# Optimization experiments

Hardware: AMD Instinct MI355X
Metric: run time of the kernel (lower is better)

The kernel has to match this reference:

```python
import jax, jax.numpy as jnp
import numpy as np

B, T, C = 4, 2048, 1024
H = 16
HD = C // H


def setup_inputs() -> dict:
    key = jax.random.key(0)
    k1, k2, k3 = jax.random.split(key, 3)
    x = jax.random.normal(k1, (B, T, C), dtype=jnp.float32)
    w_qkv = jax.random.normal(k2, (C, 3 * C), dtype=jnp.float32) * (C ** -0.5)
    w_proj = jax.random.normal(k3, (C, C), dtype=jnp.float32) * (C ** -0.5)
    b_proj = jnp.zeros((C,), dtype=jnp.float32)
    return {"x": x, "w_qkv": w_qkv, "w_proj": w_proj, "b_proj": b_proj}


def reference(x, w_qkv, w_proj, b_proj):
    Bd, Td, Cd = x.shape
    scale = HD ** -0.5
    qkv = x @ w_qkv  # [B,T,3C]
    q, k, v = jnp.split(qkv, 3, axis=-1)
    # [B,H,T,HD]
    q = q.reshape(Bd, Td, H, HD).transpose(0, 2, 1, 3)
    k = k.reshape(Bd, Td, H, HD).transpose(0, 2, 1, 3)
    v = v.reshape(Bd, Td, H, HD).transpose(0, 2, 1, 3)
    att = jnp.einsum('bhqd,bhkd->bhqk', q, k) * scale
    causal = jnp.triu(jnp.ones((Td, Td), dtype=bool), k=1)
    att = jnp.where(causal, -jnp.inf, att)
    att = jax.nn.softmax(att, axis=-1)
    y = jnp.einsum('bhqk,bhkd->bhqd', att, v)
    y = y.transpose(0, 2, 1, 3).reshape(Bd, Td, Cd)
    return y @ w_proj + b_proj
```

## Files before the change

kernel.cpp:

```cpp
#include <hip/hip_runtime.h>

typedef unsigned short u16;
typedef __attribute__((ext_vector_type(8))) short short8;
typedef __attribute__((ext_vector_type(4))) short short4v;
typedef __attribute__((ext_vector_type(4))) float floatx4;
typedef __attribute__((ext_vector_type(4))) unsigned short ushort4v;

#define B_ 4
#define T_ 2048
#define C_ 1024
#define H_ 16
#define HD_ 64

template <bool V> struct BC { static constexpr bool value = V; };
template <int N> struct ICN { static constexpr int v = N; };

static __device__ __forceinline__ u16 f2bf(float f) {
  union { float f; unsigned int i; } c; c.f = f;
  unsigned int u = c.i;
  return (u16)((u + 0x7FFFu + ((u >> 16) & 1u)) >> 16);
}
static __device__ __forceinline__ unsigned pk2(float lo, float hi) {
  union { float f; unsigned u; } a, b; a.f = hi; b.f = lo;
  return __builtin_amdgcn_perm(a.u, b.u, 0x07060302u);
}
static __device__ __forceinline__ unsigned pk2r(float lo, float hi) {
  return (unsigned)f2bf(lo) | ((unsigned)f2bf(hi) << 16);
}

static __device__ __forceinline__ void gload16(const u16* g, u16* l) {
  __builtin_amdgcn_global_load_lds(
      (const __attribute__((address_space(1))) unsigned int*)(g),
      (__attribute__((address_space(3))) unsigned int*)(l), 16, 0, 0);
}

__global__ __launch_bounds__(256) void prep_k(const float* __restrict__ x,
                                              const float* __restrict__ w_qkv,
                                              const float* __restrict__ w_proj,
                                              u16* __restrict__ xbf,
                                              u16* __restrict__ wqkvT,
                                              u16* __restrict__ wprojT) {
  const int bid = blockIdx.x;
  if (bid < 8192) {
    const int i = bid * 256 + threadIdx.x;
    const float4 f = ((const float4*)x)[i];
    ushort4v o;
    o.x = f2bf(f.x); o.y = f2bf(f.y); o.z = f2bf(f.z); o.w = f2bf(f.w);
    *(ushort4v*)(xbf + (size_t)i * 4) = o;
    return;
  }
  __shared__ u16 tile[32][33];
  const float* in;
  u16* out;
  int R, Cc, tb;
  if (bid < 11264) {
    in = w_qkv; out = wqkvT; R = C_; Cc = 3 * C_; tb = bid - 8192;
  } else {
    in = w_proj; out = wprojT; R = C_; Cc = C_; tb = bid - 11264;
  }
  const int tpr = Cc / 32;
  const int bx = (tb % tpr) * 32;
  const int by = (tb / tpr) * 32;
  const int tx = threadIdx.x & 31;
  const int ty = threadIdx.x >> 5;
  #pragma unroll
  for (int i = ty; i < 32; i += 8)
    tile[i][tx] = f2bf(in[(size_t)(by + i) * Cc + bx + tx]);
  __syncthreads();
  #pragma unroll
  for (int i = ty; i < 32; i += 8)
    out[(size_t)(bx + i) * R + by + tx] = tile[tx][i];
}

template <int MODE>
__global__ __launch_bounds__(512, 2) void gemm8p(const u16* __restrict__ A,
                                                 const u16* __restrict__ Bt,
                                                 u16* __restrict__ outb,
                                                 u16* __restrict__ outv,
                                                 float* __restrict__ outf,
                                                 const float* __restrict__ bias,
                                                 int M, int N, int K) {
  __shared__ __align__(16) u16 lds[49152];
  const int bid = blockIdx.x;
  const int xcd = bid & 7;
  const int loc = bid >> 3;
  const int tM = (xcd * 8 + (loc & 7)) * 128;
  const int tN = (loc >> 3) * 256;
  const int tid = threadIdx.x;
  const int wave = tid >> 6;
  const int lane = tid & 63;
  const int lr = lane & 15;
  const int quad = lane >> 4;
  const int wm = wave >> 2;
  const int wn = wave & 3;
  const int csw = (lr >> 1) & 3;
  const int arow = wave * 16 + (lane >> 2);
  const int skofs = ((lane & 3) ^ ((lane >> 3) & 3)) * 8;
  const int KT = K >> 5;

  const floatx4 zf = {0.f, 0.f, 0.f, 0.f};
  floatx4 acc[4][4];
  #pragma unroll
  for (int i = 0; i < 4; i++)
    #pragma unroll
    for (int j = 0; j < 4; j++) acc[i][j] = zf;

  auto stage = [&](int t) {
    const int buf = t & 3;
    const int kk = t * 32;
    gload16(A + (size_t)(tM + arow) * K + kk + skofs,
            &lds[buf * 4096 + wave * 512]);
    gload16(Bt + (size_t)(tN + arow) * K + kk + skofs,
            &lds[16384 + buf * 8192 + wave * 512]);
    gload16(Bt + (size_t)(tN + 128 + arow) * K + kk + skofs,
            &lds[16384 + buf * 8192 + 4096 + wave * 512]);
  };

  auto ktile = [&](int t, auto VM) {
    const int buf = t & 3;
    const u16* lA = &lds[buf * 4096];
    const u16* lB = &lds[16384 + buf * 8192];
    short8 af[4], bfr[4];
    #pragma unroll
    for (int mt = 0; mt < 4; mt++)
      af[mt] = *(const short8*)(&lA[(wm * 64 + mt * 16 + lr) * 32 + ((quad ^ csw) * 8)]);
    #pragma unroll
    for (int nt = 0; nt < 4; nt++)
      bfr[nt] = *(const short8*)(&lB[(wn * 64 + nt * 16 + lr) * 32 + ((quad ^ csw) * 8)]);
    if (t + 3 < KT) stage(t + 3);
    asm volatile("s_waitcnt lgkmcnt(0)" ::: "memory");
    __builtin_amdgcn_sched_barrier(0);
    __builtin_amdgcn_s_setprio(1);
    #pragma unroll
    for (int mt = 0; mt < 4; mt++)
      #pragma unroll
      for (int nt = 0; nt < 4; nt++)
        acc[mt][nt] = __builtin_amdgcn_mfma_f32_16x16x32_bf16(af[mt], bfr[nt],
                                                              acc[mt][nt], 0, 0, 0);
    __builtin_amdgcn_s_setprio(0);
    __builtin_amdgcn_sched_barrier(0);
    constexpr int vm = decltype(VM)::v;
    if constexpr (vm == 6)
      asm volatile("s_waitcnt vmcnt(6)\n\ts_barrier" ::: "memory");
    else if constexpr (vm == 3)
      asm volatile("s_waitcnt vmcnt(3)\n\ts_barrier" ::: "memory");
    else if constexpr (vm == 0)
      asm volatile("s_waitcnt vmcnt(0)\n\ts_barrier" ::: "memory");
  };

  stage(0); stage(1); stage(2);
  asm volatile("s_waitcnt vmcnt(6)\n\ts_barrier" ::: "memory");

  for (int t = 0; t < KT - 3; t++) ktile(t, ICN<6>{});
  ktile(KT - 3, ICN<3>{});
  ktile(KT - 2, ICN<0>{});
  ktile(KT - 1, ICN<-1>{});

  if constexpr (MODE == 1) {
    if (tN >= 2 * C_) {
      asm volatile("s_barrier" ::: "memory");
      #pragma unroll
      for (int mt = 0; mt < 4; mt++) {
        const int t0 = wm * 64 + mt * 16 + quad * 4;
        #pragma unroll
        for (int nt = 0; nt < 4; nt++) {
          const int vrow = wn * 64 + nt * 16 + lr;
          u16* p = &lds[vrow * 128 + (((t0 >> 3) ^ (vrow & 7)) * 8) + (t0 & 7)];
          *(unsigned*)(p)     = pk2r(acc[mt][nt][0], acc[mt][nt][1]);
          *(unsigned*)(p + 2) = pk2r(acc[mt][nt][2], acc[mt][nt][3]);
        }
      }
      asm volatile("s_waitcnt lgkmcnt(0)\n\ts_barrier" ::: "memory");
      const int b = tM >> 11;
      const int t0b = tM & (T_ - 1);
      const int h0 = (tN - 2 * C_) >> 6;
      u16* vb = outv + (size_t)(b * H_ + h0) * HD_ * T_;
      #pragma unroll
      for (int i = 0; i < 8; i++) {
        const int lin = tid + i * 512;
        const int row = lin >> 4;
        const int chv = lin & 15;
        const short8 v = *(const short8*)(&lds[row * 128 + ((chv ^ (row & 7)) * 8)]);
        *(short8*)(vb + (size_t)row * T_ + t0b + chv * 8) = v;
      }
      return;
    }
    #pragma unroll
    for (int mt = 0; mt < 4; mt++) {
      const int m0 = tM + wm * 64 + mt * 16 + quad * 4;
      #pragma unroll
      for (int nt = 0; nt < 4; nt++) {
        const int n = tN + wn * 64 + nt * 16 + lr;
        #pragma unroll
        for (int r = 0; r < 4; r++)
          outb[(size_t)(m0 + r) * N + n] = f2bf(acc[mt][nt][r]);
      }
    }
  } else {
    #pragma unroll
    for (int mt = 0; mt < 4; mt++) {
      const int m0 = tM + wm * 64 + mt * 16 + quad * 4;
      #pragma unroll
      for (int nt = 0; nt < 4; nt++) {
        const int n = tN + wn * 64 + nt * 16 + lr;
        const float bv = bias[n];
        #pragma unroll
        for (int r = 0; r < 4; r++)
          __builtin_nontemporal_store(acc[mt][nt][r] + bv,
                                      &outf[(size_t)(m0 + r) * N + n]);
      }
    }
  }
}

__global__ __launch_bounds__(256, 4) void attn_k(const u16* __restrict__ qkv,
                                                 const u16* __restrict__ vt,
                                                 u16* __restrict__ y) {
  __shared__ __align__(16) u16 Ks[64 * 64];
  __shared__ __align__(16) u16 Vs[64 * 64];
  const int bid = blockIdx.x;
  const int s = bid >> 3;
  const int qp = s >> 3;
  const int bh = ((s & 7) << 3) | (bid & 7);
  const int b = bh >> 4, h = bh & 15;
  const int tid = threadIdx.x;
  const int wave = tid >> 6;
  const int lane = tid & 63;
  const int lr = lane & 15;
  const int quad = lane >> 4;
  const int qtA = qp, qtB = 31 - qp;

  const int srow = lane >> 3;
  const int skofs = ((lane & 7) ^ ((lane >> 3) & 7)) * 8;
  const int gsw = lr & 7;

  const size_t RS = 3 * C_;
  const u16* qcol = qkv + (size_t)b * T_ * RS + h * HD_;
  const u16* kcol = qcol + C_;

  const size_t qrA = (size_t)(qtA * 64 + wave * 16 + lr) * RS;
  const size_t qrB = (size_t)(qtB * 64 + wave * 16 + lr) * RS;
  const short8 aq0A = *(const short8*)(qcol + qrA + quad * 8);
  const short8 aq1A = *(const short8*)(qcol + qrA + 32 + quad * 8);
  const short8 aq0B = *(const short8*)(qcol + qrB + quad * 8);
  const short8 aq1B = *(const short8*)(qcol + qrB + 32 + quad * 8);

  const floatx4 zf = {0.f, 0.f, 0.f, 0.f};
  const float C1 = 0.125f * 1.44269504f;
  const float C2 = -16.0f * 1.44269504f;
  const short8 vones = {16256, 16256, 16256, 16256, 16256, 16256, 16256, 16256};

  floatx4 accA[4], accB[4];
  floatx4 accSA = zf, accSB = zf;
  #pragma unroll
  for (int i = 0; i < 4; i++) { accA[i] = zf; accB[i] = zf; }

  auto stage = [&](int kt) {
    __syncthreads();
    #pragma unroll
    for (int j = 0; j < 2; j++) {
      const int seg = wave * 2 + j;
      const int row = seg * 8 + srow;
      gload16(kcol + (size_t)(kt * 64 + row) * RS + skofs, &Ks[seg * 512]);
      gload16(vt + ((size_t)bh * HD_ + row) * T_ + kt * 64 + skofs, &Vs[seg * 512]);
    }
    __syncthreads();
  };

  auto core = [&](auto WA, auto DA, auto DB) {
    constexpr bool wA = decltype(WA)::value;
    constexpr bool dA = decltype(DA)::value;
    constexpr bool dB = decltype(DB)::value;
    float peA[4][4], peB[4][4];
    #pragma unroll
    for (int nt = 0; nt < 4; nt++) {
      const short8 bk0 =
          *(const short8*)(&Ks[(nt * 16 + lr) * 64 + ((quad ^ gsw) * 8)]);
      const short8 bk1 =
          *(const short8*)(&Ks[(nt * 16 + lr) * 64 + (((quad + 4) ^ gsw) * 8)]);
      {
        floatx4 st = __builtin_amdgcn_mfma_f32_16x16x32_bf16(
            bk1, aq1B,
            __builtin_amdgcn_mfma_f32_16x16x32_bf16(bk0, aq0B, zf, 0, 0, 0),
            0, 0, 0);
        #pragma unroll
        for (int r = 0; r < 4; r++) {
          float pe = __builtin_amdgcn_exp2f(fmaf(st[r], C1, C2));
          if constexpr (dB)
            if (nt * 16 + quad * 4 + r > wave * 16 + lr) pe = 0.f;
          peB[nt][r] = pe;
        }
      }
      if constexpr (wA) {
        floatx4 st = __builtin_amdgcn_mfma_f32_16x16x32_bf16(
            bk1, aq1A,
            __builtin_amdgcn_mfma_f32_16x16x32_bf16(bk0, aq0A, zf, 0, 0, 0),
            0, 0, 0);
        #pragma unroll
        for (int r = 0; r < 4; r++) {
          float pe = __builtin_amdgcn_exp2f(fmaf(st[r], C1, C2));
          if constexpr (dA)
            if (nt * 16 + quad * 4 + r > wave * 16 + lr) pe = 0.f;
          peA[nt][r] = pe;
        }
      }
    }

    short8 pB[2], pA[2];
    #pragma unroll
    for (int h2 = 0; h2 < 2; h2++) {
      union { unsigned u[4]; short8 s8; } w;
      w.u[0] = pk2(peB[2 * h2][0], peB[2 * h2][1]);
      w.u[1] = pk2(peB[2 * h2][2], peB[2 * h2][3]);
      w.u[2] = pk2(peB[2 * h2 + 1][0], peB[2 * h2 + 1][1]);
      w.u[3] = pk2(peB[2 * h2 + 1][2], peB[2 * h2 + 1][3]);
      pB[h2] = w.s8;
    }
    if constexpr (wA) {
      #pragma unroll
      for (int h2 = 0; h2 < 2; h2++) {
        union { unsigned u[4]; short8 s8; } w;
        w.u[0] = pk2(peA[2 * h2][0], peA[2 * h2][1]);
        w.u[1] = pk2(peA[2 * h2][2], peA[2 * h2][3]);
        w.u[2] = pk2(peA[2 * h2 + 1][0], peA[2 * h2 + 1][1]);
        w.u[3] = pk2(peA[2 * h2 + 1][2], peA[2 * h2 + 1][3]);
        pA[h2] = w.s8;
      }
    }

    #pragma unroll
    for (int h2 = 0; h2 < 2; h2++) {
      accSB = __builtin_amdgcn_mfma_f32_16x16x32_bf16(vones, pB[h2], accSB, 0, 0, 0);
      if constexpr (wA)
        accSA = __builtin_amdgcn_mfma_f32_16x16x32_bf16(vones, pA[h2], accSA, 0, 0, 0);
      #pragma unroll
      for (int dt = 0; dt < 4; dt++) {
        const int base = (dt * 16 + lr) * 64;
        const int cl = h2 * 4 + (quad >> 1);
        const int off_lo = ((cl ^ gsw) * 8) + (quad & 1) * 4;
        const int off_hi = (((cl + 2) ^ gsw) * 8) + (quad & 1) * 4;
        const short4v vlo = *(const short4v*)(&Vs[base + off_lo]);
        const short4v vhi = *(const short4v*)(&Vs[base + off_hi]);
        const short8 av = __builtin_shufflevector(vlo, vhi, 0, 1, 2, 3, 4, 5, 6, 7);
        accB[dt] = __builtin_amdgcn_mfma_f32_16x16x32_bf16(av, pB[h2], accB[dt], 0, 0, 0);
        if constexpr (wA)
          accA[dt] = __builtin_amdgcn_mfma_f32_16x16x32_bf16(av, pA[h2], accA[dt], 0, 0, 0);
      }
    }
  };

  for (int kt = 0; kt < qtA; kt++) { stage(kt); core(BC<true>{}, BC<false>{}, BC<false>{}); }
  stage(qtA); core(BC<true>{}, BC<true>{}, BC<false>{});
  for (int kt = qtA + 1; kt < qtB; kt++) { stage(kt); core(BC<false>{}, BC<false>{}, BC<false>{}); }
  stage(qtB); core(BC<false>{}, BC<false>{}, BC<true>{});

  #pragma unroll
  for (int ph = 0; ph < 2; ph++) {
    const int qt = ph ? qtB : qtA;
    const floatx4* acc = ph ? accB : accA;
    const float inv = 1.f / (ph ? accSB[0] : accSA[0]);
    const int qg = qt * 64 + wave * 16 + lr;
    u16* yrow = y + ((size_t)(b * T_ + qg)) * C_ + h * HD_;
    #pragma unroll
    for (int dt = 0; dt < 4; dt++) {
      ushort4v o;
      #pragma unroll
      for (int r = 0; r < 4; r++) o[r] = f2bf(acc[dt][r] * inv);
      *(ushort4v*)(yrow + dt * 16 + quad * 4) = o;
    }
  }
}

extern "C" void kernel_launch(void* const* d_in, const int* in_sizes, int n_in,
                              void* d_out, int out_size, void* d_ws, size_t ws_size,
                              hipStream_t stream) {
  const float* x      = (const float*)d_in[0];
  const float* w_qkv  = (const float*)d_in[1];
  const float* w_proj = (const float*)d_in[2];
  const float* b_proj = (const float*)d_in[3];
  float* out = (float*)d_out;

  u16* ws = (u16*)d_ws;
  const size_t SZ = (size_t)B_ * T_ * C_;
  u16* xbf    = ws;
  u16* wqkvT  = xbf + SZ;
  u16* wprojT = wqkvT + (size_t)3 * C_ * C_;
  u16* qkvw   = wprojT + (size_t)C_ * C_;
  u16* vtw    = qkvw + 3 * SZ;
  u16* yw     = xbf;

  prep_k<<<12288, 256, 0, stream>>>(x, w_qkv, w_proj, xbf, wqkvT, wprojT);
  gemm8p<1><<<768, 512, 0, stream>>>(
      xbf, wqkvT, qkvw, vtw, nullptr, nullptr, B_ * T_, 3 * C_, C_);
  attn_k<<<1024, 256, 0, stream>>>(qkvw, vtw, yw);
  gemm8p<2><<<256, 512, 0, stream>>>(
      yw, wprojT, nullptr, nullptr, out, b_proj, B_ * T_, C_, C_);
}
```

Baseline: 235.7 us.

## Restructure GEMMs to four-wave blocks with triple-buffered K pipeline

Replaces the 8-wave GEMM with a 4-wave kernel in which each wave computes a 64x(16*NFR) tile. The QKV projection keeps a 128x256 block tile, while the output projection now uses 128x128 tiles across twice as many blocks. The prefetch pipeline drops from four LDS buffers to three, with precomputed per-wave load addresses and K fixed at 1024. The explicit lgkmcnt waits and scheduling barriers are removed, and the compiler is left to order LDS reads and MFMAs. The aim is better per-wave MFMA reuse and occupancy, with more output-projection blocks to fill the device. The cost is higher register pressure and a shallower prefetch depth.

Measured after the change: 229.7 us. 1.03x faster.

```diff
diff --git a/kernel.cpp b/kernel.cpp
--- a/kernel.cpp
+++ b/kernel.cpp
@@ -32,6 +32,15 @@
   __builtin_amdgcn_global_load_lds(
       (const __attribute__((address_space(1))) unsigned int*)(g),
       (__attribute__((address_space(3))) unsigned int*)(l), 16, 0, 0);
+}
+
+template <int N> static __device__ __forceinline__ void wait_vm_bar() {
+  if constexpr (N == 6)
+    asm volatile("s_waitcnt vmcnt(6)\n\ts_barrier" ::: "memory");
+  else if constexpr (N == 4)
+    asm volatile("s_waitcnt vmcnt(4)\n\ts_barrier" ::: "memory");
+  else if constexpr (N == 0)
+    asm volatile("s_waitcnt vmcnt(0)\n\ts_barrier" ::: "memory");
 }
 
 __global__ __launch_bounds__(256) void prep_k(const float* __restrict__ x,
@@ -72,89 +81,99 @@
     out[(size_t)(bx + i) * R + by + tx] = tile[tx][i];
 }
 
-template <int MODE>
-__global__ __launch_bounds__(512, 2) void gemm8p(const u16* __restrict__ A,
+template <int MODE, int NFR>
+__global__ __launch_bounds__(256, 2) void gemm4w(const u16* __restrict__ A,
                                                  const u16* __restrict__ Bt,
                                                  u16* __restrict__ outb,
                                                  u16* __restrict__ outv,
                                                  float* __restrict__ outf,
                                                  const float* __restrict__ bias,
-                                                 int M, int N, int K) {
-  __shared__ __align__(16) u16 lds[49152];
+                                                 int M, int N) {
+  constexpr int TN = NFR * 32;
+  constexpr int BUFA = 4096;
+  constexpr int BUFB = TN * 32;
+  constexpr int BUF = BUFA + BUFB;
+  constexpr int LPW = (8 + TN / 16) / 4;
+  __shared__ __align__(16) u16 lds[3 * BUF];
+
   const int bid = blockIdx.x;
   const int xcd = bid & 7;
   const int loc = bid >> 3;
   const int tM = (xcd * 8 + (loc & 7)) * 128;
-  const int tN = (loc >> 3) * 256;
+  const int tN = (loc >> 3) * TN;
   const int tid = threadIdx.x;
   const int wave = tid >> 6;
   const int lane = tid & 63;
   const int lr = lane & 15;
   const int quad = lane >> 4;
-  const int wm = wave >> 2;
-  const int wn = wave & 3;
+  const int wm = wave >> 1;
+  const int wn = wave & 1;
   const int csw = (lr >> 1) & 3;
-  const int arow = wave * 16 + (lane >> 2);
+  const int srow = lane >> 2;
   const int skofs = ((lane & 3) ^ ((lane >> 3) & 3)) * 8;
-  const int KT = K >> 5;
+
+  const u16* gbase[LPW];
+  int ldst[LPW];
+  #pragma unroll
+  for (int j = 0; j < LPW; j++) {
+    const int s = wave * LPW + j;
+    if (s < 8) {
+      gbase[j] = A + (size_t)(tM + s * 16 + srow) * 1024 + skofs;
+      ldst[j] = s * 512;
+    } else {
+      gbase[j] = Bt + (size_t)(tN + (s - 8) * 16 + srow) * 1024 + skofs;
+      ldst[j] = BUFA + (s - 8) * 512;
+    }
+  }
 
   const floatx4 zf = {0.f, 0.f, 0.f, 0.f};
-  floatx4 acc[4][4];
+  floatx4 acc[4][NFR];
   #pragma unroll
   for (int i = 0; i < 4; i++)
     #pragma unroll
-    for (int j = 0; j < 4; j++) acc[i][j] = zf;
-
-  auto stage = [&](int t) {
-    const int buf = t & 3;
-    const int kk = t * 32;
-    gload16(A + (size_t)(tM + arow) * K + kk + skofs,
-            &lds[buf * 4096 + wave * 512]);
-    gload16(Bt + (size_t)(tN + arow) * K + kk + skofs,
-            &lds[16384 + buf * 8192 + wave * 512]);
-    gload16(Bt + (size_t)(tN + 128 + arow) * K + kk + skofs,
-            &lds[16384 + buf * 8192 + 4096 + wave * 512]);
+    for (int j = 0; j < NFR; j++) acc[i][j] = zf;
+
+  auto stage = [&](int t, int buf) {
+    #pragma unroll
+    for (int j = 0; j < LPW; j++)
+      gload16(gbase[j] + t * 32, &lds[buf * BUF + ldst[j]]);
   };
 
-  auto ktile = [&](int t, auto VM) {
-    const int buf = t & 3;
-    const u16* lA = &lds[buf * 4096];
-    const u16* lB = &lds[16384 + buf * 8192];
-    short8 af[4], bfr[4];
+  auto ktile = [&](int t, int buf, auto VM) {
+    constexpr int vm = decltype(VM)::v;
+    const u16* lA = &lds[buf * BUF];
+    const u16* lB = lA + BUFA;
+    short8 af[4], bfr[NFR];
     #pragma unroll
     for (int mt = 0; mt < 4; mt++)
       af[mt] = *(const short8*)(&lA[(wm * 64 + mt * 16 + lr) * 32 + ((quad ^ csw) * 8)]);
     #pragma unroll
-    for (int nt = 0; nt < 4; nt++)
-      bfr[nt] = *(const short8*)(&lB[(wn * 64 + nt * 16 + lr) * 32 + ((quad ^ csw) * 8)]);
-    if (t + 3 < KT) stage(t + 3);
-    asm volatile("s_waitcnt lgkmcnt(0)" ::: "memory");
-    __builtin_amdgcn_sched_barrier(0);
+    for (int nt = 0; nt < NFR; nt++)
+      bfr[nt] = *(const short8*)(&lB[(wn * (NFR * 16) + nt * 16 + lr) * 32 + ((quad ^ csw) * 8)]);
+    if constexpr (vm > 0) stage(t + 2, (buf + 2) % 3);
     __builtin_amdgcn_s_setprio(1);
     #pragma unroll
     for (int mt = 0; mt < 4; mt++)
       #pragma unroll
-      for (int nt = 0; nt < 4; nt++)
+      for (int nt = 0; nt < NFR; nt++)
         acc[mt][nt] = __builtin_amdgcn_mfma_f32_16x16x32_bf16(af[mt], bfr[nt],
                                                               acc[mt][nt], 0, 0, 0);
     __builtin_amdgcn_s_setprio(0);
-    __builtin_amdgcn_sched_barrier(0);
-    constexpr int vm = decltype(VM)::v;
-    if constexpr (vm == 6)
-      asm volatile("s_waitcnt vmcnt(6)\n\ts_barrier" ::: "memory");
-    else if constexpr (vm == 3)
-      asm volatile("s_waitcnt vmcnt(3)\n\ts_barrier" ::: "memory");
-    else if constexpr (vm == 0)
-      asm volatile("s_waitcnt vmcnt(0)\n\ts_barrier" ::: "memory");
+    if constexpr (vm > 0) wait_vm_bar<LPW>();
+    else if constexpr (vm == 0) wait_vm_bar<0>();
   };
 
-  stage(0); stage(1); stage(2);
-  asm volatile("s_waitcnt vmcnt(6)\n\ts_barrier" ::: "memory");
-
-  for (int t = 0; t < KT - 3; t++) ktile(t, ICN<6>{});
-  ktile(KT - 3, ICN<3>{});
-  ktile(KT - 2, ICN<0>{});
-  ktile(KT - 1, ICN<-1>{});
+  stage(0, 0); stage(1, 1);
+  wait_vm_bar<LPW>();
+
+  for (int tb = 0; tb < 10; ++tb) {
+    const int t = tb * 3;
+    ktile(t,     0, ICN<LPW>{});
+    ktile(t + 1, 1, ICN<LPW>{});
+    ktile(t + 2, 2, ICN<LPW>{});
+  }
+  ktile(30, 0, ICN<0>{});
+  ktile(31, 1, ICN<-1>{});
 
   if constexpr (MODE == 1) {
     if (tN >= 2 * C_) {
@@ -163,8 +182,8 @@
       for (int mt = 0; mt < 4; mt++) {
         const int t0 = wm * 64 + mt * 16 + quad * 4;
         #pragma unroll
-        for (int nt = 0; nt < 4; nt++) {
-          const int vrow = wn * 64 + nt * 16 + lr;
+        for (int nt = 0; nt < NFR; nt++) {
+          const int vrow = wn * (NFR * 16) + nt * 16 + lr;
           u16* p = &lds[vrow * 128 + (((t0 >> 3) ^ (vrow & 7)) * 8) + (t0 & 7)];
           *(unsigned*)(p)     = pk2r(acc[mt][nt][0], acc[mt][nt][1]);
           *(unsigned*)(p + 2) = pk2r(acc[mt][nt][2], acc[mt][nt][3]);
@@ -176,8 +195,8 @@
       const int h0 = (tN - 2 * C_) >> 6;
       u16* vb = outv + (size_t)(b * H_ + h0) * HD_ * T_;
       #pragma unroll
-      for (int i = 0; i < 8; i++) {
-        const int lin = tid + i * 512;
+      for (int i = 0; i < 16; i++) {
+        const int lin = tid + i * 256;
         const int row = lin >> 4;
         const int chv = lin & 15;
         const short8 v = *(const short8*)(&lds[row * 128 + ((chv ^ (row & 7)) * 8)]);
@@ -189,8 +208,8 @@
     for (int mt = 0; mt < 4; mt++) {
       const int m0 = tM + wm * 64 + mt * 16 + quad * 4;
       #pragma unroll
-      for (int nt = 0; nt < 4; nt++) {
-        const int n = tN + wn * 64 + nt * 16 + lr;
+      for (int nt = 0; nt < NFR; nt++) {
+        const int n = tN + wn * (NFR * 16) + nt * 16 + lr;
         #pragma unroll
         for (int r = 0; r < 4; r++)
           outb[(size_t)(m0 + r) * N + n] = f2bf(acc[mt][nt][r]);
@@ -201,8 +220,8 @@
     for (int mt = 0; mt < 4; mt++) {
       const int m0 = tM + wm * 64 + mt * 16 + quad * 4;
       #pragma unroll
-      for (int nt = 0; nt < 4; nt++) {
-        const int n = tN + wn * 64 + nt * 16 + lr;
+      for (int nt = 0; nt < NFR; nt++) {
+        const int n = tN + wn * (NFR * 16) + nt * 16 + lr;
         const float bv = bias[n];
         #pragma unroll
         for (int r = 0; r < 4; r++)
@@ -390,9 +409,9 @@
   u16* yw     = xbf;
 
   prep_k<<<12288, 256, 0, stream>>>(x, w_qkv, w_proj, xbf, wqkvT, wprojT);
-  gemm8p<1><<<768, 512, 0, stream>>>(
-      xbf, wqkvT, qkvw, vtw, nullptr, nullptr, B_ * T_, 3 * C_, C_);
+  gemm4w<1, 8><<<768, 256, 0, stream>>>(
+      xbf, wqkvT, qkvw, vtw, nullptr, nullptr, B_ * T_, 3 * C_);
   attn_k<<<1024, 256, 0, stream>>>(qkvw, vtw, yw);
-  gemm8p<2><<<256, 512, 0, stream>>>(
-      yw, wprojT, nullptr, nullptr, out, b_proj, B_ * T_, C_, C_);
-}
+  gemm4w<2, 4><<<512, 256, 0, stream>>>(
+      yw, wprojT, nullptr, nullptr, out, b_proj, B_ * T_, C_);
+}
```

## Restructure GEMM pipeline to double-buffered 64-wide K tiles with split phases

Applied to the files above, without the earlier changes.

Replaces the 4-deep, 32-wide K-tile LDS ring in the GEMM with a 2-deep buffer of 64-wide K tiles. Each tile is consumed in two half-phases, and the next tile's half is prefetched during each phase. K is hardcoded to 1024 with precomputed global pointers. Launch bounds drop to one block per CU, which gives more registers but less occupancy. An extra barrier per phase and the shallower prefetch could expose memory latency.

Measured after the change: 231.1 us. 2.0% less time.

```diff
diff --git a/kernel.cpp b/kernel.cpp
--- a/kernel.cpp
+++ b/kernel.cpp
@@ -73,14 +73,16 @@
 }
 
 template <int MODE>
-__global__ __launch_bounds__(512, 2) void gemm8p(const u16* __restrict__ A,
-                                                 const u16* __restrict__ Bt,
-                                                 u16* __restrict__ outb,
-                                                 u16* __restrict__ outv,
-                                                 float* __restrict__ outf,
-                                                 const float* __restrict__ bias,
-                                                 int M, int N, int K) {
-  __shared__ __align__(16) u16 lds[49152];
+__global__ __launch_bounds__(512, 1)
+void gemm8x(const u16* __restrict__ A, const u16* __restrict__ Bt,
+            u16* __restrict__ outb, u16* __restrict__ outv,
+            float* __restrict__ outf, const float* __restrict__ bias,
+            int N) {
+  constexpr int ABUF = 8192;
+  constexpr int BBUF = 16384;
+  constexpr int BUF = ABUF + BBUF;
+  __shared__ __align__(16) u16 lds[2 * BUF];
+
   const int bid = blockIdx.x;
   const int xcd = bid & 7;
   const int loc = bid >> 3;
@@ -94,9 +96,15 @@
   const int wm = wave >> 2;
   const int wn = wave & 3;
   const int csw = (lr >> 1) & 3;
-  const int arow = wave * 16 + (lane >> 2);
+  const int srow = lane >> 2;
   const int skofs = ((lane & 3) ^ ((lane >> 3) & 3)) * 8;
-  const int KT = K >> 5;
+
+  const u16* gA  = A  + (size_t)(tM + wave * 16 + srow) * 1024 + skofs;
+  const u16* gB0 = Bt + (size_t)(tN + (wave * 2) * 16 + srow) * 1024 + skofs;
+  const u16* gB1 = Bt + (size_t)(tN + (wave * 2 + 1) * 16 + srow) * 1024 + skofs;
+  u16* lA  = &lds[wave * 512];
+  u16* lB0 = &lds[ABUF + (wave * 2) * 512];
+  u16* lB1 = &lds[ABUF + (wave * 2 + 1) * 512];
 
   const floatx4 zf = {0.f, 0.f, 0.f, 0.f};
   floatx4 acc[4][4];
@@ -105,29 +113,27 @@
     #pragma unroll
     for (int j = 0; j < 4; j++) acc[i][j] = zf;
 
-  auto stage = [&](int t) {
-    const int buf = t & 3;
-    const int kk = t * 32;
-    gload16(A + (size_t)(tM + arow) * K + kk + skofs,
-            &lds[buf * 4096 + wave * 512]);
-    gload16(Bt + (size_t)(tN + arow) * K + kk + skofs,
-            &lds[16384 + buf * 8192 + wave * 512]);
-    gload16(Bt + (size_t)(tN + 128 + arow) * K + kk + skofs,
-            &lds[16384 + buf * 8192 + 4096 + wave * 512]);
+  auto stage = [&](int t, int kh) {
+    const int buf = t & 1;
+    const int go = t * 64 + kh * 32;
+    gload16(gA + go,  lA  + buf * BUF + kh * 4096);
+    gload16(gB0 + go, lB0 + buf * BUF + kh * 8192);
+    gload16(gB1 + go, lB1 + buf * BUF + kh * 8192);
   };
 
-  auto ktile = [&](int t, auto VM) {
-    const int buf = t & 3;
-    const u16* lA = &lds[buf * 4096];
-    const u16* lB = &lds[16384 + buf * 8192];
-    short8 af[4], bfr[4];
+  auto phase = [&](int t, int kh, auto STG, auto VM) {
+    const int buf = t & 1;
+    const u16* pA = &lds[buf * BUF + kh * 4096];
+    const u16* pB = &lds[buf * BUF + ABUF + kh * 8192];
+    short8 af[4], bf[4];
     #pragma unroll
     for (int mt = 0; mt < 4; mt++)
-      af[mt] = *(const short8*)(&lA[(wm * 64 + mt * 16 + lr) * 32 + ((quad ^ csw) * 8)]);
+      af[mt] = *(const short8*)(&pA[(wm * 64 + mt * 16 + lr) * 32 + ((quad ^ csw) * 8)]);
     #pragma unroll
     for (int nt = 0; nt < 4; nt++)
-      bfr[nt] = *(const short8*)(&lB[(wn * 64 + nt * 16 + lr) * 32 + ((quad ^ csw) * 8)]);
-    if (t + 3 < KT) stage(t + 3);
+      bf[nt] = *(const short8*)(&pB[(wn * 64 + nt * 16 + lr) * 32 + ((quad ^ csw) * 8)]);
+    if constexpr (decltype(STG)::value) stage(t + 1, kh);
+    asm volatile("s_barrier" ::: "memory");
     asm volatile("s_waitcnt lgkmcnt(0)" ::: "memory");
     __builtin_amdgcn_sched_barrier(0);
     __builtin_amdgcn_s_setprio(1);
@@ -135,30 +141,32 @@
     for (int mt = 0; mt < 4; mt++)
       #pragma unroll
       for (int nt = 0; nt < 4; nt++)
-        acc[mt][nt] = __builtin_amdgcn_mfma_f32_16x16x32_bf16(af[mt], bfr[nt],
+        acc[mt][nt] = __builtin_amdgcn_mfma_f32_16x16x32_bf16(af[mt], bf[nt],
                                                               acc[mt][nt], 0, 0, 0);
     __builtin_amdgcn_s_setprio(0);
-    __builtin_amdgcn_sched_barrier(0);
     constexpr int vm = decltype(VM)::v;
-    if constexpr (vm == 6)
-      asm volatile("s_waitcnt vmcnt(6)\n\ts_barrier" ::: "memory");
-    else if constexpr (vm == 3)
+    if constexpr (vm == 3)
       asm volatile("s_waitcnt vmcnt(3)\n\ts_barrier" ::: "memory");
     else if constexpr (vm == 0)
       asm volatile("s_waitcnt vmcnt(0)\n\ts_barrier" ::: "memory");
+    else
+      asm volatile("s_barrier" ::: "memory");
   };
 
-  stage(0); stage(1); stage(2);
-  asm volatile("s_waitcnt vmcnt(6)\n\ts_barrier" ::: "memory");
-
-  for (int t = 0; t < KT - 3; t++) ktile(t, ICN<6>{});
-  ktile(KT - 3, ICN<3>{});
-  ktile(KT - 2, ICN<0>{});
-  ktile(KT - 1, ICN<-1>{});
+  stage(0, 0);
+  stage(0, 1);
+  asm volatile("s_waitcnt vmcnt(3)\n\ts_barrier" ::: "memory");
+
+  #pragma unroll 1
+  for (int t = 0; t < 15; t++) {
+    phase(t, 0, BC<true>{}, ICN<3>{});
+    phase(t, 1, BC<true>{}, ICN<3>{});
+  }
+  phase(15, 0, BC<false>{}, ICN<0>{});
+  phase(15, 1, BC<false>{}, ICN<-1>{});
 
   if constexpr (MODE == 1) {
     if (tN >= 2 * C_) {
-      asm volatile("s_barrier" ::: "memory");
       #pragma unroll
       for (int mt = 0; mt < 4; mt++) {
         const int t0 = wm * 64 + mt * 16 + quad * 4;
@@ -390,9 +398,9 @@
   u16* yw     = xbf;
 
   prep_k<<<12288, 256, 0, stream>>>(x, w_qkv, w_proj, xbf, wqkvT, wprojT);
-  gemm8p<1><<<768, 512, 0, stream>>>(
-      xbf, wqkvT, qkvw, vtw, nullptr, nullptr, B_ * T_, 3 * C_, C_);
+  gemm8x<1><<<768, 512, 0, stream>>>(
+      xbf, wqkvT, qkvw, vtw, nullptr, nullptr, 3 * C_);
   attn_k<<<1024, 256, 0, stream>>>(qkvw, vtw, yw);
-  gemm8p<2><<<256, 512, 0, stream>>>(
-      yw, wprojT, nullptr, nullptr, out, b_proj, B_ * T_, C_, C_);
-}
+  gemm8x<2><<<256, 512, 0, stream>>>(
+      yw, wprojT, nullptr, nullptr, out, b_proj, C_);
+}
```
